# Kernel tuning notes

Measured on AMD Instinct MI355X. Metric: run time of the kernel, lower is better.

Reference implementation:

```python
import jax, jax.numpy as jnp
import numpy as np

N = 32768      # nodes
E = 524288     # edges (avg degree 16)
F = 64         # node_feat_dim
D = 64         # gnn_dim (= per-head out channels, concat=False)
ED = 32        # edge_feat_dim
L = 6          # num_layers
H = 2          # heads
C = D          # per-head channels
LN_EPS = 1e-5


def layer_norm(h, g, b):
    mu = jnp.mean(h, axis=-1, keepdims=True)
    var = jnp.mean((h - mu) ** 2, axis=-1, keepdims=True)
    return g * (h - mu) * jax.lax.rsqrt(var + LN_EPS) + b


def setup_inputs() -> dict:
    key = jax.random.key(0)
    ks = jax.random.split(key, 16)
    x = jax.random.normal(ks[0], (N, F), jnp.float32)
    edge_index = jax.random.randint(ks[1], (2, E), 0, N, jnp.int32)
    edge_attr = jax.random.normal(ks[2], (E, ED), jnp.float32)
    manual_gamma = 1.0 + 0.1 * jax.random.normal(ks[3], (L, D), jnp.float32)
    manual_beta = 0.1 * jax.random.normal(ks[4], (L, D), jnp.float32)
    # node_embed Linear(F, D)
    embed_W = jax.random.normal(ks[5], (F, D), jnp.float32) / np.float32(np.sqrt(F))
    embed_b = jnp.zeros((D,), jnp.float32)
    # per-layer LayerNorm affine params
    ln_gamma = jnp.ones((L, D), jnp.float32)
    ln_beta = jnp.zeros((L, D), jnp.float32)
    # per-layer GATConv params (shared lin for src/dst, PyG non-bipartite)
    lin_W = jax.random.normal(ks[6], (L, D, H * C), jnp.float32) / np.float32(np.sqrt(D))
    lin_edge_W = jax.random.normal(ks[7], (L, ED, H * C), jnp.float32) / np.float32(np.sqrt(ED))
    att_src = jax.random.normal(ks[8], (L, H, C), jnp.float32) / np.float32(np.sqrt(C))
    att_dst = jax.random.normal(ks[9], (L, H, C), jnp.float32) / np.float32(np.sqrt(C))
    att_edge = jax.random.normal(ks[10], (L, H, C), jnp.float32) / np.float32(np.sqrt(C))
    gat_bias = jnp.zeros((L, C), jnp.float32)
    # edge output head: Linear(2D+ED, D) -> ReLU -> Linear(D, 1)
    head_W1 = jax.random.normal(ks[11], (2 * D + ED, D), jnp.float32) / np.float32(np.sqrt(2 * D + ED))
    head_b1 = jnp.zeros((D,), jnp.float32)
    head_W2 = jax.random.normal(ks[12], (D, 1), jnp.float32) / np.float32(np.sqrt(D))
    head_b2 = jnp.zeros((1,), jnp.float32)
    return dict(x=x, edge_index=edge_index, edge_attr=edge_attr,
                manual_gamma=manual_gamma, manual_beta=manual_beta,
                embed_W=embed_W, embed_b=embed_b, ln_gamma=ln_gamma, ln_beta=ln_beta,
                lin_W=lin_W, lin_edge_W=lin_edge_W, att_src=att_src, att_dst=att_dst,
                att_edge=att_edge, gat_bias=gat_bias, head_W1=head_W1, head_b1=head_b1,
                head_W2=head_W2, head_b2=head_b2)


def reference(x, edge_index, edge_attr, manual_gamma, manual_beta,
              embed_W, embed_b, ln_gamma, ln_beta, lin_W, lin_edge_W,
              att_src, att_dst, att_edge, gat_bias, head_W1, head_b1,
              head_W2, head_b2):
    src, dst = edge_index[0], edge_index[1]
    # PyG GATConv default add_self_loops=True, fill_value='mean' for edge_attr
    loop = jnp.arange(N, dtype=edge_index.dtype)
    src_f = jnp.concatenate([src, loop])   # [E+N]
    dst_f = jnp.concatenate([dst, loop])
    deg = jax.ops.segment_sum(jnp.ones((E,), x.dtype), dst, num_segments=N)
    loop_attr = jax.ops.segment_sum(edge_attr, dst, num_segments=N) / jnp.maximum(deg, 1.0)[:, None]
    edge_attr_f = jnp.concatenate([edge_attr, loop_attr], axis=0)  # [E+N, ED]

    h = x @ embed_W + embed_b  # [N, D]
    for l in range(L):
        hn = layer_norm(h, ln_gamma[l], ln_beta[l])
        hm = manual_gamma[l][None, :] * hn + manual_beta[l][None, :]
        xh = (hm @ lin_W[l]).reshape(N, H, C)                      # [N,H,C]
        a_s = jnp.sum(xh * att_src[l][None], axis=-1)              # [N,H]
        a_d = jnp.sum(xh * att_dst[l][None], axis=-1)              # [N,H]
        eh = (edge_attr_f @ lin_edge_W[l]).reshape(-1, H, C)       # [E+N,H,C]
        a_e = jnp.sum(eh * att_edge[l][None], axis=-1)             # [E+N,H]
        alpha = jax.nn.leaky_relu(a_s[src_f] + a_d[dst_f] + a_e, 0.2)
        amax = jax.ops.segment_max(alpha, dst_f, num_segments=N)   # every node has a self-loop
        ex = jnp.exp(alpha - amax[dst_f])
        den = jax.ops.segment_sum(ex, dst_f, num_segments=N)
        w = ex / (den[dst_f] + 1e-16)                              # segment softmax [E+N,H]
        msg = xh[src_f] * w[..., None]                             # [E+N,H,C]
        out = jax.ops.segment_sum(msg, dst_f, num_segments=N)      # [N,H,C]
        h = jax.nn.relu(jnp.mean(out, axis=1) + gat_bias[l])       # concat=False -> head mean

    ef = jnp.concatenate([h[src], h[dst], edge_attr], axis=-1)     # [E, 2D+ED]
    hid = jax.nn.relu(ef @ head_W1 + head_b1)
    return (hid @ head_W2 + head_b2)[:, 0]                         # [E]
```

## Files before the change

kernel.cpp:

```cpp
#include <hip/hip_runtime.h>
#include <hip/hip_bf16.h>
#include <math.h>

#define NN 32768
#define EE 524288
#define LL 6

typedef __attribute__((ext_vector_type(8))) short short8;
typedef __attribute__((ext_vector_type(4))) float floatx4;

union U16x8 { short8 v; unsigned short u[8]; };

__device__ __forceinline__ unsigned short f2bf(float x) {
    union { float f; unsigned int u; } v; v.f = x;
    unsigned int r = v.u + 0x7fffu + ((v.u >> 16) & 1u);
    return (unsigned short)(r >> 16);
}
__device__ __forceinline__ float bf2f(unsigned short h) {
    union { unsigned int u; float f; } v; v.u = (unsigned int)h << 16;
    return v.f;
}


__global__ __launch_bounds__(1024) void scan_kernel(const int* __restrict__ deg,
                                                    int* __restrict__ row_ptr,
                                                    int* __restrict__ cnt) {
    __shared__ int bs[1024];
    int t = threadIdx.x;
    int base = t * 32;
    int loc[32];
    int s = 0;
#pragma unroll
    for (int i = 0; i < 32; ++i) { int v = deg[base + i]; loc[i] = s; s += v; }
    bs[t] = s;
    __syncthreads();
    for (int off = 1; off < 1024; off <<= 1) {
        int v = (t >= off) ? bs[t - off] : 0;
        __syncthreads();
        bs[t] += v;
        __syncthreads();
    }
    int pre = (t == 0) ? 0 : bs[t - 1];
#pragma unroll
    for (int i = 0; i < 32; ++i) { row_ptr[base + i] = pre + loc[i]; cnt[base + i] = 0; }
    if (t == 1023) row_ptr[NN] = bs[1023];
}

__global__ void fill_kernel(const int* __restrict__ src, const int* __restrict__ dst,
                            const int* __restrict__ row_ptr, int* __restrict__ cnt,
                            int2* __restrict__ sedge) {
    int e = blockIdx.x * 256 + threadIdx.x;
    if (e >= EE) return;
    int d = dst[e];
    int pos = row_ptr[d] + atomicAdd(&cnt[d], 1);
    sedge[pos] = make_int2(src[e], e);
}

__global__ __launch_bounds__(256) void smallprep_kernel(
    const float* __restrict__ lin_W, const float* __restrict__ head_W1,
    const float* __restrict__ lin_edge_W, const float* __restrict__ att_edge,
    const float* __restrict__ att_src, const float* __restrict__ att_dst,
    unsigned short* __restrict__ gBhi, unsigned short* __restrict__ gBlo,
    float* __restrict__ vbuf, float* __restrict__ vs, float* __restrict__ vvd,
    unsigned short* __restrict__ w1chi, unsigned short* __restrict__ w1clo) {
    int bb = blockIdx.x;
    int tid = threadIdx.x;
    if (bb < 7) {
        unsigned short* dh = gBhi + (size_t)bb * 128 * 64;
        unsigned short* dl = gBlo + (size_t)bb * 128 * 64;
        if (bb < 6) {
            int n2 = tid & 63, kh = tid >> 6;
            U16x8 hh[4], ll[4];
            for (int kk = 0; kk < 32; ++kk) {
                int j = kh * 32 + kk;
                int h = j >> 6, k = j & 63;
                float wv = 0.5f * lin_W[((size_t)bb * 64 + k) * 128 + h * 64 + n2];
                unsigned short h16 = f2bf(wv);
                hh[kk >> 3].u[kk & 7] = h16;
                ll[kk >> 3].u[kk & 7] = f2bf(wv - bf2f(h16));
            }
#pragma unroll
            for (int c = 0; c < 4; ++c) {
                int cg = kh * 4 + c;
                int off = n2 * 128 + ((cg ^ (n2 & 15)) << 3);
                *(short8*)(dh + off) = hh[c].v;
                *(short8*)(dl + off) = ll[c].v;
            }
        } else {
            int n = tid & 127, kh = tid >> 7;
            U16x8 hh[4], ll[4];
            for (int kk = 0; kk < 32; ++kk) {
                int k = kh * 32 + kk;
                float wv = (n < 64) ? head_W1[k * 64 + n] : head_W1[(64 + k) * 64 + (n - 64)];
                unsigned short h16 = f2bf(wv);
                hh[kk >> 3].u[kk & 7] = h16;
                ll[kk >> 3].u[kk & 7] = f2bf(wv - bf2f(h16));
            }
#pragma unroll
            for (int c = 0; c < 4; ++c) {
                int cg = kh * 4 + c;
                int off = n * 64 + ((cg ^ (n & 7)) << 3);
                *(short8*)(dh + off) = hh[c].v;
                *(short8*)(dl + off) = ll[c].v;
            }
        }
    } else if (bb == 7) {
        for (int t = tid; t < 384; t += 256) {
            int l = t / 64; int r = t & 63; int ed = r >> 1; int hh = r & 1;
            const float* w = lin_edge_W + l * 32 * 128 + ed * 128 + hh * 64;
            const float* a = att_edge + l * 128 + hh * 64;
            float s = 0.f;
#pragma unroll 8
            for (int c = 0; c < 64; ++c) s += w[c] * a[c];
            vbuf[t] = s;
        }
        int n = tid & 63, kc = tid >> 6;
#pragma unroll
        for (int j = 0; j < 8; ++j) {
            int k = kc * 8 + j;
            float wv = head_W1[(128 + k) * 64 + n];
            unsigned short h16 = f2bf(wv);
            w1chi[n * 32 + k] = h16;
            w1clo[n * 32 + k] = f2bf(wv - bf2f(h16));
        }
    } else {
        int l = bb - 8;
        int sel = tid >> 7, idx = tid & 127;
        int h = idx >> 6, k = idx & 63;
        const float* att = (sel ? att_dst : att_src) + l * 128 + h * 64;
        const float* wr = lin_W + ((size_t)l * 64 + k) * 128 + h * 64;
        float s = 0.f;
#pragma unroll 8
        for (int c = 0; c < 64; ++c) s += wr[c] * att[c];
        (sel ? vvd : vs)[l * 128 + idx] = s;
    }
}

__global__ void ae_deg_kernel(const float* __restrict__ edge_attr,
                              const int* __restrict__ dst,
                              const float* __restrict__ v,
                              float* __restrict__ aeo,
                              unsigned short* __restrict__ eabf,
                              int* __restrict__ deg) {
    __shared__ float sv[384];
    int tid = threadIdx.x;
    for (int i = tid; i < 384; i += 128) sv[i] = v[i];
    __syncthreads();
    int e = blockIdx.x * 128 + tid;
    if (e >= EE) return;
    atomicAdd(&deg[dst[e]], 1);
    float ea[32];
    const float4* p = (const float4*)(edge_attr + (size_t)e * 32);
#pragma unroll
    for (int i = 0; i < 8; ++i) {
        float4 f = p[i];
        ea[4 * i] = f.x; ea[4 * i + 1] = f.y; ea[4 * i + 2] = f.z; ea[4 * i + 3] = f.w;
    }
    U16x8 ub[4];
#pragma unroll
    for (int j = 0; j < 32; ++j) ub[j >> 3].u[j & 7] = f2bf(ea[j]);
#pragma unroll
    for (int j = 0; j < 4; ++j) *(short8*)(eabf + (size_t)e * 32 + j * 8) = ub[j].v;
#pragma unroll
    for (int l = 0; l < LL; ++l) {
        float s0 = 0.f, s1 = 0.f;
#pragma unroll
        for (int ed = 0; ed < 32; ++ed) {
            float x = ea[ed];
            s0 += x * sv[l * 64 + ed * 2];
            s1 += x * sv[l * 64 + ed * 2 + 1];
        }
        aeo[((size_t)l * EE + e) * 2] = s0;
        aeo[((size_t)l * EE + e) * 2 + 1] = s1;
    }
}

__global__ __launch_bounds__(256) void embed_ln_kernel(
    const float* __restrict__ x, const float* __restrict__ W, const float* __restrict__ b,
    const float* __restrict__ ln_g, const float* __restrict__ ln_b,
    const float* __restrict__ mg, const float* __restrict__ mb,
    const float* __restrict__ vs0, const float* __restrict__ vd0,
    unsigned short* __restrict__ hm_bf, float* __restrict__ a_s, float* __restrict__ a_d) {
    __shared__ float xr[4][64];
    int w = threadIdx.x >> 6, j = threadIdx.x & 63;
    int n = blockIdx.x * 4 + w;
    xr[w][j] = x[(size_t)n * 64 + j];
    __syncthreads();
    float acc = b[j];
#pragma unroll 8
    for (int k = 0; k < 64; ++k) acc += xr[w][k] * W[k * 64 + j];
    float s = acc, sq = acc * acc;
    for (int off = 1; off < 64; off <<= 1) { s += __shfl_xor(s, off); sq += __shfl_xor(sq, off); }
    float mu = s * (1.f / 64.f);
    float var = sq * (1.f / 64.f) - mu * mu;
    float rs = rsqrtf(var + 1e-5f);
    float hm = mg[j] * (ln_g[j] * (acc - mu) * rs + ln_b[j]) + mb[j];
    hm_bf[(size_t)n * 64 + j] = f2bf(hm);
    float s0 = hm * vs0[j], s1 = hm * vs0[64 + j];
    float d0 = hm * vd0[j], d1 = hm * vd0[64 + j];
    for (int off = 1; off < 64; off <<= 1) {
        s0 += __shfl_xor(s0, off); s1 += __shfl_xor(s1, off);
        d0 += __shfl_xor(d0, off); d1 += __shfl_xor(d1, off);
    }
    if (j == 0) {
        a_s[n * 2] = s0; a_s[n * 2 + 1] = s1;
        a_d[n * 2] = d0; a_d[n * 2 + 1] = d1;
    }
}

__device__ __forceinline__ void fma8(uint4 pv, float w0, float w1, float* a0, float* a1) {
    unsigned int u[4] = {pv.x, pv.y, pv.z, pv.w};
#pragma unroll
    for (int j = 0; j < 4; ++j) {
        union { unsigned int q; float f; } lo, hi;
        lo.q = u[j] << 16; hi.q = u[j] & 0xffff0000u;
        a0[2 * j] += w0 * lo.f;  a1[2 * j] += w1 * lo.f;
        a0[2 * j + 1] += w0 * hi.f;  a1[2 * j + 1] += w1 * hi.f;
    }
}

__global__ __launch_bounds__(256) void aggregate6_kernel(
    const unsigned short* __restrict__ hm_bf, const float* __restrict__ a_s,
    const float* __restrict__ a_d, const float* __restrict__ aeo,
    const int* __restrict__ row_ptr, const int2* __restrict__ sedge,
    unsigned short* __restrict__ Abf) {
    int w = threadIdx.x >> 6, lane = threadIdx.x & 63;
    int n = blockIdx.x * 4 + w;
    int slot = lane >> 3, ch = lane & 7;
    const float2* as2 = (const float2*)a_s;
    const float2* ae2 = (const float2*)aeo;
    const uint4* hmv = (const uint4*)hm_bf;
    float2 adn = ((const float2*)a_d)[n];
    float2 asn = as2[n];
    uint4 pvself = hmv[(size_t)n * 8 + ch];
    int beg = row_ptr[n], end = row_ptr[n + 1];

    float acc0[8] = {}, acc1[8] = {};
    float den0 = 0.f, den1 = 0.f, aex = 0.f, aey = 0.f;

    for (int cs = beg; cs < end; cs += 64) {
        int cnt = min(64, end - cs);
        float w0v = 0.f, w1v = 0.f;
        int sval = n;
        if (lane < cnt) {
            int2 se = sedge[cs + lane];
            float2 ae = ae2[se.y];
            float2 as = as2[se.x];
            aex += ae.x; aey += ae.y;
            float al0 = as.x + adn.x + ae.x; al0 = al0 > 0.f ? al0 : 0.2f * al0;
            float al1 = as.y + adn.y + ae.y; al1 = al1 > 0.f ? al1 : 0.2f * al1;
            w0v = __expf(al0);
            w1v = __expf(al1);
            sval = se.x;
        }
        int ng2 = (cnt + 15) >> 4;
        for (int g2 = 0; g2 < ng2; ++g2) {
            int eA = g2 * 16 + slot, eB = eA + 8;
            int svA = __shfl(sval, eA), svB = __shfl(sval, eB);
            float wA0 = __shfl(w0v, eA), wA1 = __shfl(w1v, eA);
            float wB0 = __shfl(w0v, eB), wB1 = __shfl(w1v, eB);
            uint4 pvA = hmv[(size_t)svA * 8 + ch];
            uint4 pvB = hmv[(size_t)svB * 8 + ch];
            fma8(pvA, wA0, wA1, acc0, acc1);
            den0 += wA0; den1 += wA1;
            fma8(pvB, wB0, wB1, acc0, acc1);
            den0 += wB0; den1 += wB1;
        }
    }
    for (int m = 1; m < 8; m <<= 1) {
        aex += __shfl_xor(aex, m);
        aey += __shfl_xor(aey, m);
    }
#pragma unroll
    for (int m = 8; m < 64; m <<= 1) {
#pragma unroll
        for (int j = 0; j < 8; ++j) {
            acc0[j] += __shfl_xor(acc0[j], m);
            acc1[j] += __shfl_xor(acc1[j], m);
        }
        den0 += __shfl_xor(den0, m);
        den1 += __shfl_xor(den1, m);
        aex += __shfl_xor(aex, m);
        aey += __shfl_xor(aey, m);
    }
    if (slot == 0) {
        float invd = 1.f / fmaxf((float)(end - beg), 1.f);
        float al0 = asn.x + adn.x + aex * invd; al0 = al0 > 0.f ? al0 : 0.2f * al0;
        float al1 = asn.y + adn.y + aey * invd; al1 = al1 > 0.f ? al1 : 0.2f * al1;
        float ws0 = __expf(al0), ws1 = __expf(al1);
        fma8(pvself, ws0, ws1, acc0, acc1);
        den0 += ws0; den1 += ws1;
        float inv0 = 1.f / (den0 + 1e-16f), inv1 = 1.f / (den1 + 1e-16f);
        U16x8 h0, h1;
#pragma unroll
        for (int j = 0; j < 8; ++j) {
            h0.u[j] = f2bf(acc0[j] * inv0);
            h1.u[j] = f2bf(acc1[j] * inv1);
        }
        int i15 = n & 15;
        unsigned short* row = Abf + (size_t)n * 128;
        *(short8*)(row + ((ch ^ i15) << 3)) = h0.v;
        *(short8*)(row + (((8 + ch) ^ i15) << 3)) = h1.v;
    }
}

__global__ __launch_bounds__(256) void post_gemm(
    const unsigned short* __restrict__ Abf, const unsigned short* __restrict__ gBhi,
    const unsigned short* __restrict__ gBlo, const float* __restrict__ bias,
    const float* __restrict__ ln_g, const float* __restrict__ ln_b,
    const float* __restrict__ mg, const float* __restrict__ mb,
    const float* __restrict__ vsn, const float* __restrict__ vdn,
    unsigned short* __restrict__ hm_bf, float* __restrict__ a_s, float* __restrict__ a_d) {
    __shared__ unsigned short Ahi[64 * 128];
    __shared__ unsigned short Bhi[64 * 128], Blo[64 * 128];
    int tid = threadIdx.x;
    {
        const uint4* sa = (const uint4*)(Abf + (size_t)blockIdx.x * 64 * 128);
        const uint4* sh = (const uint4*)gBhi;
        const uint4* sl = (const uint4*)gBlo;
        for (int i = tid; i < 1024; i += 256) {
            ((uint4*)Ahi)[i] = sa[i];
            ((uint4*)Bhi)[i] = sh[i];
            ((uint4*)Blo)[i] = sl[i];
        }
    }
    __syncthreads();

    int w = tid >> 6, lane = tid & 63, col = lane & 15, quad = lane >> 4;
    int m = w * 16 + col;
    floatx4 acc[4] = {};
#pragma unroll
    for (int s = 0; s < 4; ++s) {
        int ca = (quad + 4 * s) ^ col;
        short8 ahi = *(const short8*)(Ahi + m * 128 + ca * 8);
#pragma unroll
        for (int t = 0; t < 4; ++t) {
            int off = (t * 16 + col) * 128 + ca * 8;
            short8 bhi = *(const short8*)(Bhi + off);
            short8 blo = *(const short8*)(Blo + off);
            acc[t] = __builtin_amdgcn_mfma_f32_16x16x32_bf16(ahi, blo, acc[t], 0, 0, 0);
            acc[t] = __builtin_amdgcn_mfma_f32_16x16x32_bf16(ahi, bhi, acc[t], 0, 0, 0);
        }
    }
    int nodebase = blockIdx.x * 64 + w * 16;
    float bv[4];
#pragma unroll
    for (int t = 0; t < 4; ++t) bv[t] = bias[t * 16 + col];
    float vsv[4], vsv1[4], vdv[4], vdv1[4], lg[4], lb[4], mgv[4], mbv[4];
#pragma unroll
    for (int t = 0; t < 4; ++t) {
        int c = t * 16 + col;
        vsv[t] = vsn[c]; vsv1[t] = vsn[64 + c];
        vdv[t] = vdn[c]; vdv1[t] = vdn[64 + c];
        lg[t] = ln_g[c]; lb[t] = ln_b[c];
        mgv[t] = mg[c]; mbv[t] = mb[c];
    }
#pragma unroll
    for (int r = 0; r < 4; ++r) {
        int node = nodebase + quad * 4 + r;
        float hv[4];
        float s = 0.f, sq = 0.f;
#pragma unroll
        for (int t = 0; t < 4; ++t) {
            float v = acc[t][r] + bv[t];
            v = v > 0.f ? v : 0.f;
            hv[t] = v;
            s += v; sq += v * v;
        }
        for (int off = 1; off < 16; off <<= 1) { s += __shfl_xor(s, off); sq += __shfl_xor(sq, off); }
        float mu = s * (1.f / 64.f);
        float var = sq * (1.f / 64.f) - mu * mu;
        float rs = rsqrtf(var + 1e-5f);
        float s0 = 0.f, s1 = 0.f, d0 = 0.f, d1 = 0.f;
#pragma unroll
        for (int t = 0; t < 4; ++t) {
            float hmv = mgv[t] * (lg[t] * (hv[t] - mu) * rs + lb[t]) + mbv[t];
            hm_bf[(size_t)node * 64 + t * 16 + col] = f2bf(hmv);
            s0 += hmv * vsv[t]; s1 += hmv * vsv1[t];
            d0 += hmv * vdv[t]; d1 += hmv * vdv1[t];
        }
        for (int off = 1; off < 16; off <<= 1) {
            s0 += __shfl_xor(s0, off); s1 += __shfl_xor(s1, off);
            d0 += __shfl_xor(d0, off); d1 += __shfl_xor(d1, off);
        }
        if (col == 0) {
            a_s[node * 2] = s0; a_s[node * 2 + 1] = s1;
            a_d[node * 2] = d0; a_d[node * 2 + 1] = d1;
        }
    }
}

__global__ __launch_bounds__(256) void postuv_gemm(
    const unsigned short* __restrict__ Abf, const unsigned short* __restrict__ gB5hi,
    const unsigned short* __restrict__ gB5lo, const float* __restrict__ bias,
    const unsigned short* __restrict__ gB6hi, const unsigned short* __restrict__ gB6lo,
    unsigned short* __restrict__ uv) {
    __shared__ unsigned short lds[24576];
    unsigned short* Ahi  = lds;
    unsigned short* B5hi = lds + 8192;
    unsigned short* B5lo = lds + 16384;
    unsigned short* A2hi = lds;
    unsigned short* A2lo = lds + 4096;
    unsigned short* B6hi = lds + 8192;
    unsigned short* B6lo = lds + 16384;
    int tid = threadIdx.x;
    {
        const uint4* sa = (const uint4*)(Abf + (size_t)blockIdx.x * 64 * 128);
        const uint4* sh = (const uint4*)gB5hi;
        const uint4* sl = (const uint4*)gB5lo;
        for (int i = tid; i < 1024; i += 256) {
            ((uint4*)Ahi)[i] = sa[i];
            ((uint4*)B5hi)[i] = sh[i];
            ((uint4*)B5lo)[i] = sl[i];
        }
    }
    __syncthreads();

    int w = tid >> 6, lane = tid & 63, col = lane & 15, quad = lane >> 4;
    int m = w * 16 + col;
    floatx4 acc[4] = {};
#pragma unroll
    for (int s = 0; s < 4; ++s) {
        int ca = (quad + 4 * s) ^ col;
        short8 ahi = *(const short8*)(Ahi + m * 128 + ca * 8);
#pragma unroll
        for (int t = 0; t < 4; ++t) {
            int off = (t * 16 + col) * 128 + ca * 8;
            short8 bhi = *(const short8*)(B5hi + off);
            short8 blo = *(const short8*)(B5lo + off);
            acc[t] = __builtin_amdgcn_mfma_f32_16x16x32_bf16(ahi, blo, acc[t], 0, 0, 0);
            acc[t] = __builtin_amdgcn_mfma_f32_16x16x32_bf16(ahi, bhi, acc[t], 0, 0, 0);
        }
    }
    float bv[4];
#pragma unroll
    for (int t = 0; t < 4; ++t) bv[t] = bias[t * 16 + col];
    __syncthreads();
#pragma unroll
    for (int t = 0; t < 4; ++t) {
        int c = t * 16 + col;
        int cg = c >> 3, cr = c & 7;
#pragma unroll
        for (int r = 0; r < 4; ++r) {
            float v = acc[t][r] + bv[t];
            v = v > 0.f ? v : 0.f;
            int i = w * 16 + quad * 4 + r;
            int off = i * 64 + ((cg ^ (i & 7)) << 3) + cr;
            unsigned short hh = f2bf(v);
            A2hi[off] = hh;
            A2lo[off] = f2bf(v - bf2f(hh));
        }
    }
    for (int i = tid; i < 1024; i += 256) {
        ((uint4*)B6hi)[i] = ((const uint4*)gB6hi)[i];
        ((uint4*)B6lo)[i] = ((const uint4*)gB6lo)[i];
    }
    __syncthreads();

    floatx4 acc2[8] = {};
#pragma unroll
    for (int s = 0; s < 2; ++s) {
        int ca = (quad + 4 * s) ^ (col & 7);
        short8 a2h = *(const short8*)(A2hi + m * 64 + ca * 8);
        short8 a2l = *(const short8*)(A2lo + m * 64 + ca * 8);
#pragma unroll
        for (int t = 0; t < 8; ++t) {
            int off = (t * 16 + col) * 64 + ca * 8;
            short8 bh = *(const short8*)(B6hi + off);
            short8 bl = *(const short8*)(B6lo + off);
            acc2[t] = __builtin_amdgcn_mfma_f32_16x16x32_bf16(a2l, bh, acc2[t], 0, 0, 0);
            acc2[t] = __builtin_amdgcn_mfma_f32_16x16x32_bf16(a2h, bl, acc2[t], 0, 0, 0);
            acc2[t] = __builtin_amdgcn_mfma_f32_16x16x32_bf16(a2h, bh, acc2[t], 0, 0, 0);
        }
    }
    int nodebase = blockIdx.x * 64 + w * 16;
#pragma unroll
    for (int t = 0; t < 8; ++t)
#pragma unroll
        for (int r = 0; r < 4; ++r)
            uv[(size_t)(nodebase + quad * 4 + r) * 128 + t * 16 + col] = f2bf(acc2[t][r]);
}

__global__ __launch_bounds__(256) void head2_kernel(
    const unsigned short* __restrict__ uv, const int* __restrict__ src,
    const int* __restrict__ dst, const unsigned short* __restrict__ eabf,
    const unsigned short* __restrict__ w1chi, const unsigned short* __restrict__ w1clo,
    const float* __restrict__ b1, const float* __restrict__ W2,
    const float* __restrict__ b2, float* __restrict__ out) {
    __shared__ float g[64][68];
    __shared__ unsigned short Abf[64 * 40];
    __shared__ unsigned short Bh[64 * 40], Bl[64 * 40];
    __shared__ int sA[64], dA[64];
    int tid = threadIdx.x;
    int base = blockIdx.x * 64;
    if (tid < 64) sA[tid] = src[base + tid];
    else if (tid < 128) dA[tid - 64] = dst[base + tid - 64];
    {
        int n = tid >> 2, c = tid & 3;
        *(short8*)(Bh + n * 40 + c * 8) = *(const short8*)(w1chi + n * 32 + c * 8);
        *(short8*)(Bl + n * 40 + c * 8) = *(const short8*)(w1clo + n * 32 + c * 8);
    }
    {
        int e = tid >> 2, q = tid & 3;
        *(short8*)(Abf + e * 40 + q * 8) = *(const short8*)(eabf + (size_t)(base + e) * 32 + q * 8);
    }
    __syncthreads();
    {
        int e = tid >> 2, q = tid & 3;
        const uint4* su = (const uint4*)(uv + (size_t)sA[e] * 128);
        const uint4* dv = (const uint4*)(uv + (size_t)dA[e] * 128);
        uint4 U0 = su[2 * q], U1 = su[2 * q + 1];
        uint4 V0 = dv[8 + 2 * q], V1 = dv[9 + 2 * q];
        const float4* b1p = (const float4*)(b1 + q * 16);
        float bb[16];
#pragma unroll
        for (int j = 0; j < 4; ++j) {
            float4 b4 = b1p[j];
            bb[4 * j] = b4.x; bb[4 * j + 1] = b4.y; bb[4 * j + 2] = b4.z; bb[4 * j + 3] = b4.w;
        }
        unsigned int uw[8] = {U0.x, U0.y, U0.z, U0.w, U1.x, U1.y, U1.z, U1.w};
        unsigned int vw[8] = {V0.x, V0.y, V0.z, V0.w, V1.x, V1.y, V1.z, V1.w};
        float* gr = &g[e][q * 16];
#pragma unroll
        for (int j = 0; j < 8; ++j) {
            gr[2 * j] = bf2f((unsigned short)(uw[j] & 0xffff)) +
                        bf2f((unsigned short)(vw[j] & 0xffff)) + bb[2 * j];
            gr[2 * j + 1] = bf2f((unsigned short)(uw[j] >> 16)) +
                            bf2f((unsigned short)(vw[j] >> 16)) + bb[2 * j + 1];
        }
    }
    __syncthreads();

    int lane = tid & 63, w = tid >> 6, col = lane & 15, quad = lane >> 4;
    short8 a = *(const short8*)(Abf + (w * 16 + col) * 40 + quad * 8);
    floatx4 acc[4] = {};
#pragma unroll
    for (int t = 0; t < 4; ++t) {
        int off = (t * 16 + col) * 40 + quad * 8;
        short8 bh = *(const short8*)(Bh + off);
        short8 bl = *(const short8*)(Bl + off);
        acc[t] = __builtin_amdgcn_mfma_f32_16x16x32_bf16(a, bl, acc[t], 0, 0, 0);
        acc[t] = __builtin_amdgcn_mfma_f32_16x16x32_bf16(a, bh, acc[t], 0, 0, 0);
    }
    float sv[4] = {0.f, 0.f, 0.f, 0.f};
#pragma unroll
    for (int t = 0; t < 4; ++t) {
        float w2v = W2[t * 16 + col];
#pragma unroll
        for (int r = 0; r < 4; ++r) {
            float hid = acc[t][r] + g[w * 16 + quad * 4 + r][t * 16 + col];
            hid = hid > 0.f ? hid : 0.f;
            sv[r] += hid * w2v;
        }
    }
    float b2v = b2[0];
#pragma unroll
    for (int r = 0; r < 4; ++r) {
        float v = sv[r];
        v += __shfl_xor(v, 1);
        v += __shfl_xor(v, 2);
        v += __shfl_xor(v, 4);
        v += __shfl_xor(v, 8);
        if (col == 0) out[base + w * 16 + quad * 4 + r] = v + b2v;
    }
}


extern "C" void kernel_launch(void* const* d_in, const int* in_sizes, int n_in,
                              void* d_out, int out_size, void* d_ws, size_t ws_size,
                              hipStream_t stream) {
    const float* x            = (const float*)d_in[0];
    const int*   edge_index   = (const int*)d_in[1];
    const float* edge_attr    = (const float*)d_in[2];
    const float* manual_gamma = (const float*)d_in[3];
    const float* manual_beta  = (const float*)d_in[4];
    const float* embed_W      = (const float*)d_in[5];
    const float* embed_b      = (const float*)d_in[6];
    const float* ln_gamma     = (const float*)d_in[7];
    const float* ln_beta      = (const float*)d_in[8];
    const float* lin_W        = (const float*)d_in[9];
    const float* lin_edge_W   = (const float*)d_in[10];
    const float* att_src      = (const float*)d_in[11];
    const float* att_dst      = (const float*)d_in[12];
    const float* att_edge     = (const float*)d_in[13];
    const float* gat_bias     = (const float*)d_in[14];
    const float* head_W1      = (const float*)d_in[15];
    const float* head_b1      = (const float*)d_in[16];
    const float* head_W2      = (const float*)d_in[17];
    const float* head_b2      = (const float*)d_in[18];
    float* out = (float*)d_out;

    const int* src = edge_index;
    const int* dst = edge_index + EE;

    char* ws = (char*)d_ws;
    size_t off = 0;
    auto alloc = [&](size_t bytes) {
        void* p = ws + off;
        off += (bytes + 255) & ~(size_t)255;
        return p;
    };
    int*   deg        = (int*)alloc(NN * 4);
    int*   row_ptr    = (int*)alloc((NN + 1) * 4);
    int*   cnt        = (int*)alloc(NN * 4);
    int2*  sedge      = (int2*)alloc((size_t)EE * 8);
    float* aeo        = (float*)alloc((size_t)LL * EE * 2 * 4);
    float* vbuf       = (float*)alloc(LL * 64 * 4);
    float* vs         = (float*)alloc(LL * 128 * 4);
    float* vvd        = (float*)alloc(LL * 128 * 4);
    float* a_s        = (float*)alloc((size_t)NN * 2 * 4);
    float* a_d        = (float*)alloc((size_t)NN * 2 * 4);
    unsigned short* Abf   = (unsigned short*)alloc((size_t)NN * 128 * 2);
    unsigned short* hm_bf = (unsigned short*)alloc((size_t)NN * 64 * 2);
    unsigned short* uvbuf = (unsigned short*)alloc((size_t)NN * 128 * 2);
    unsigned short* eabf  = (unsigned short*)alloc((size_t)EE * 32 * 2);
    unsigned short* gBhi  = (unsigned short*)alloc((size_t)7 * 128 * 64 * 2);
    unsigned short* gBlo  = (unsigned short*)alloc((size_t)7 * 128 * 64 * 2);
    unsigned short* w1chi = (unsigned short*)alloc(64 * 32 * 2);
    unsigned short* w1clo = (unsigned short*)alloc(64 * 32 * 2);
    if (off > ws_size) return;

    hipMemsetAsync(deg, 0, NN * 4, stream);

    smallprep_kernel<<<14, 256, 0, stream>>>(lin_W, head_W1, lin_edge_W, att_edge,
                                             att_src, att_dst, gBhi, gBlo, vbuf,
                                             vs, vvd, w1chi, w1clo);
    ae_deg_kernel<<<EE / 128, 128, 0, stream>>>(edge_attr, dst, vbuf, aeo, eabf, deg);
    scan_kernel<<<1, 1024, 0, stream>>>(deg, row_ptr, cnt);
    fill_kernel<<<EE / 256, 256, 0, stream>>>(src, dst, row_ptr, cnt, sedge);
    embed_ln_kernel<<<NN / 4, 256, 0, stream>>>(x, embed_W, embed_b, ln_gamma, ln_beta,
                                                manual_gamma, manual_beta, vs, vvd,
                                                hm_bf, a_s, a_d);

    for (int l = 0; l < LL; ++l) {
        aggregate6_kernel<<<NN / 4, 256, 0, stream>>>(
            hm_bf, a_s, a_d, aeo + (size_t)l * EE * 2, row_ptr, sedge, Abf);
        if (l < LL - 1) {
            post_gemm<<<NN / 64, 256, 0, stream>>>(
                Abf, gBhi + (size_t)l * 128 * 64, gBlo + (size_t)l * 128 * 64,
                gat_bias + l * 64, ln_gamma + (l + 1) * 64, ln_beta + (l + 1) * 64,
                manual_gamma + (l + 1) * 64, manual_beta + (l + 1) * 64,
                vs + (l + 1) * 128, vvd + (l + 1) * 128, hm_bf, a_s, a_d);
        } else {
            postuv_gemm<<<NN / 64, 256, 0, stream>>>(
                Abf, gBhi + (size_t)l * 128 * 64, gBlo + (size_t)l * 128 * 64,
                gat_bias + l * 64, gBhi + (size_t)6 * 128 * 64,
                gBlo + (size_t)6 * 128 * 64, uvbuf);
        }
    }

    head2_kernel<<<EE / 64, 256, 0, stream>>>(uvbuf, src, dst, eabf, w1chi, w1clo,
                                              head_b1, head_W2, head_b2, out);
}
```

Measured before the change: 511.9 us.

## Compute edge attention logits with split-bf16 MFMA and aggregate four nodes per wave

The per-edge attention-logit precompute in ae_deg_kernel moves from scalar FMAs to three bf16 MFMA ops on hi/lo split operands, with the small weight matrix packed in smallprep. The aggregation kernel now assigns 16 lanes per destination node, so one wave handles four nodes, each lane covers one head by 8 channels, and the cross-slot shuffle reduction goes away. This aims to cut idle lanes on low-degree nodes and reduce reduction overhead. In exchange, the wave loops to the maximum degree among its four nodes, and the split-bf16 MFMA adds small numeric differences.

```diff
diff --git a/kernel.cpp b/kernel.cpp
--- a/kernel.cpp
+++ b/kernel.cpp
@@ -61,8 +61,10 @@
     const float* __restrict__ lin_edge_W, const float* __restrict__ att_edge,
     const float* __restrict__ att_src, const float* __restrict__ att_dst,
     unsigned short* __restrict__ gBhi, unsigned short* __restrict__ gBlo,
-    float* __restrict__ vbuf, float* __restrict__ vs, float* __restrict__ vvd,
+    unsigned short* __restrict__ aeBhi, unsigned short* __restrict__ aeBlo,
+    float* __restrict__ vs, float* __restrict__ vvd,
     unsigned short* __restrict__ w1chi, unsigned short* __restrict__ w1clo) {
+    __shared__ float svb[384];
     int bb = blockIdx.x;
     int tid = threadIdx.x;
     if (bb < 7) {
@@ -112,7 +114,7 @@
             float s = 0.f;
 #pragma unroll 8
             for (int c = 0; c < 64; ++c) s += w[c] * a[c];
-            vbuf[t] = s;
+            svb[t] = s;
         }
         int n = tid & 63, kc = tid >> 6;
 #pragma unroll
@@ -122,6 +124,21 @@
             unsigned short h16 = f2bf(wv);
             w1chi[n * 32 + k] = h16;
             w1clo[n * 32 + k] = f2bf(wv - bf2f(h16));
+        }
+        __syncthreads();
+        if (tid < 64) {
+            int n2 = tid & 15, q = tid >> 4;
+            U16x8 hi, lo;
+#pragma unroll
+            for (int i = 0; i < 8; ++i) {
+                int k = q * 8 + i;
+                float val = (n2 < 12) ? svb[(n2 >> 1) * 64 + k * 2 + (n2 & 1)] : 0.f;
+                unsigned short h16 = f2bf(val);
+                hi.u[i] = h16;
+                lo.u[i] = f2bf(val - bf2f(h16));
+            }
+            *(short8*)(aeBhi + tid * 8) = hi.v;
+            *(short8*)(aeBlo + tid * 8) = lo.v;
         }
     } else {
         int l = bb - 8;
@@ -136,42 +153,45 @@
     }
 }
 
-__global__ void ae_deg_kernel(const float* __restrict__ edge_attr,
-                              const int* __restrict__ dst,
-                              const float* __restrict__ v,
-                              float* __restrict__ aeo,
-                              unsigned short* __restrict__ eabf,
-                              int* __restrict__ deg) {
-    __shared__ float sv[384];
+__global__ __launch_bounds__(256) void ae_deg_kernel(
+    const float* __restrict__ edge_attr, const int* __restrict__ dst,
+    const unsigned short* __restrict__ aeBhi, const unsigned short* __restrict__ aeBlo,
+    float* __restrict__ aeo, unsigned short* __restrict__ eabf, int* __restrict__ deg) {
     int tid = threadIdx.x;
-    for (int i = tid; i < 384; i += 128) sv[i] = v[i];
-    __syncthreads();
-    int e = blockIdx.x * 128 + tid;
-    if (e >= EE) return;
+    int w = tid >> 6, lane = tid & 63;
+    int e0 = blockIdx.x * 256 + w * 64;
+    int e = blockIdx.x * 256 + tid;
     atomicAdd(&deg[dst[e]], 1);
-    float ea[32];
-    const float4* p = (const float4*)(edge_attr + (size_t)e * 32);
-#pragma unroll
-    for (int i = 0; i < 8; ++i) {
-        float4 f = p[i];
-        ea[4 * i] = f.x; ea[4 * i + 1] = f.y; ea[4 * i + 2] = f.z; ea[4 * i + 3] = f.w;
-    }
-    U16x8 ub[4];
-#pragma unroll
-    for (int j = 0; j < 32; ++j) ub[j >> 3].u[j & 7] = f2bf(ea[j]);
-#pragma unroll
-    for (int j = 0; j < 4; ++j) *(short8*)(eabf + (size_t)e * 32 + j * 8) = ub[j].v;
-#pragma unroll
-    for (int l = 0; l < LL; ++l) {
-        float s0 = 0.f, s1 = 0.f;
-#pragma unroll
-        for (int ed = 0; ed < 32; ++ed) {
-            float x = ea[ed];
-            s0 += x * sv[l * 64 + ed * 2];
-            s1 += x * sv[l * 64 + ed * 2 + 1];
-        }
-        aeo[((size_t)l * EE + e) * 2] = s0;
-        aeo[((size_t)l * EE + e) * 2 + 1] = s1;
+    short8 bhi = *(const short8*)(aeBhi + lane * 8);
+    short8 blo = *(const short8*)(aeBlo + lane * 8);
+    int r = lane & 15, q = lane >> 4;
+#pragma unroll
+    for (int t = 0; t < 4; ++t) {
+        int er = e0 + t * 16 + r;
+        const float4* p = (const float4*)(edge_attr + (size_t)er * 32 + q * 8);
+        float4 f0 = p[0], f1 = p[1];
+        float av[8] = {f0.x, f0.y, f0.z, f0.w, f1.x, f1.y, f1.z, f1.w};
+        U16x8 hi, lo;
+#pragma unroll
+        for (int jj = 0; jj < 8; ++jj) {
+            unsigned short h16 = f2bf(av[jj]);
+            hi.u[jj] = h16;
+            lo.u[jj] = f2bf(av[jj] - bf2f(h16));
+        }
+        *(short8*)(eabf + (size_t)er * 32 + q * 8) = hi.v;
+        floatx4 acc = {};
+        acc = __builtin_amdgcn_mfma_f32_16x16x32_bf16(lo.v, bhi, acc, 0, 0, 0);
+        acc = __builtin_amdgcn_mfma_f32_16x16x32_bf16(hi.v, blo, acc, 0, 0, 0);
+        acc = __builtin_amdgcn_mfma_f32_16x16x32_bf16(hi.v, bhi, acc, 0, 0, 0);
+        if (r < 12) {
+            int l = r >> 1, h = r & 1;
+            float* dstp = aeo + (size_t)l * EE * 2 + h;
+#pragma unroll
+            for (int rr = 0; rr < 4; ++rr) {
+                int ee2 = e0 + t * 16 + q * 4 + rr;
+                dstp[(size_t)ee2 * 2] = acc[rr];
+            }
+        }
     }
 }
 
@@ -208,25 +228,26 @@
     }
 }
 
-__device__ __forceinline__ void fma8(uint4 pv, float w0, float w1, float* a0, float* a1) {
+__device__ __forceinline__ void fma8h(uint4 pv, float w, float* a) {
     unsigned int u[4] = {pv.x, pv.y, pv.z, pv.w};
 #pragma unroll
-    for (int j = 0; j < 4; ++j) {
-        union { unsigned int q; float f; } lo, hi;
-        lo.q = u[j] << 16; hi.q = u[j] & 0xffff0000u;
-        a0[2 * j] += w0 * lo.f;  a1[2 * j] += w1 * lo.f;
-        a0[2 * j + 1] += w0 * hi.f;  a1[2 * j + 1] += w1 * hi.f;
-    }
-}
-
-__global__ __launch_bounds__(256) void aggregate6_kernel(
+    for (int q = 0; q < 4; ++q) {
+        union { unsigned int x; float f; } lo, hi;
+        lo.x = u[q] << 16; hi.x = u[q] & 0xffff0000u;
+        a[2 * q]     += w * lo.f;
+        a[2 * q + 1] += w * hi.f;
+    }
+}
+
+__global__ __launch_bounds__(256) void aggregate7_kernel(
     const unsigned short* __restrict__ hm_bf, const float* __restrict__ a_s,
     const float* __restrict__ a_d, const float* __restrict__ aeo,
     const int* __restrict__ row_ptr, const int2* __restrict__ sedge,
     unsigned short* __restrict__ Abf) {
     int w = threadIdx.x >> 6, lane = threadIdx.x & 63;
-    int n = blockIdx.x * 4 + w;
-    int slot = lane >> 3, ch = lane & 7;
+    int g = lane >> 4, j = lane & 15;
+    int ch = j & 7, hh = j >> 3;
+    int n = blockIdx.x * 16 + w * 4 + g;
     const float2* as2 = (const float2*)a_s;
     const float2* ae2 = (const float2*)aeo;
     const uint4* hmv = (const uint4*)hm_bf;
@@ -234,16 +255,25 @@
     float2 asn = as2[n];
     uint4 pvself = hmv[(size_t)n * 8 + ch];
     int beg = row_ptr[n], end = row_ptr[n + 1];
-
-    float acc0[8] = {}, acc1[8] = {};
-    float den0 = 0.f, den1 = 0.f, aex = 0.f, aey = 0.f;
-
-    for (int cs = beg; cs < end; cs += 64) {
-        int cnt = min(64, end - cs);
+    int degn = end - beg;
+
+    float acc[8] = {};
+    float den = 0.f, aex = 0.f, aey = 0.f;
+    int gbase = g << 4;
+
+    int niter = (degn + 15) >> 4;
+    {
+        int o = __shfl_xor(niter, 16); niter = niter > o ? niter : o;
+        o = __shfl_xor(niter, 32); niter = niter > o ? niter : o;
+    }
+    for (int it = 0; it < niter; ++it) {
+        int cs = beg + (it << 4);
+        int rem = end - cs;
+        rem = rem > 16 ? 16 : rem;
         float w0v = 0.f, w1v = 0.f;
         int sval = n;
-        if (lane < cnt) {
-            int2 se = sedge[cs + lane];
+        if (j < rem) {
+            int2 se = sedge[cs + j];
             float2 ae = ae2[se.y];
             float2 as = as2[se.x];
             aex += ae.x; aey += ae.y;
@@ -253,55 +283,39 @@
             w1v = __expf(al1);
             sval = se.x;
         }
-        int ng2 = (cnt + 15) >> 4;
-        for (int g2 = 0; g2 < ng2; ++g2) {
-            int eA = g2 * 16 + slot, eB = eA + 8;
-            int svA = __shfl(sval, eA), svB = __shfl(sval, eB);
-            float wA0 = __shfl(w0v, eA), wA1 = __shfl(w1v, eA);
-            float wB0 = __shfl(w0v, eB), wB1 = __shfl(w1v, eB);
-            uint4 pvA = hmv[(size_t)svA * 8 + ch];
-            uint4 pvB = hmv[(size_t)svB * 8 + ch];
-            fma8(pvA, wA0, wA1, acc0, acc1);
-            den0 += wA0; den1 += wA1;
-            fma8(pvB, wB0, wB1, acc0, acc1);
-            den0 += wB0; den1 += wB1;
-        }
-    }
-    for (int m = 1; m < 8; m <<= 1) {
+        int r2 = rem > 0 ? rem : 0;
+        {
+            int o = __shfl_xor(r2, 16); r2 = r2 > o ? r2 : o;
+            o = __shfl_xor(r2, 32); r2 = r2 > o ? r2 : o;
+        }
+        for (int s = 0; s < r2; ++s) {
+            int idx = gbase + s;
+            int sb = __shfl(sval, idx);
+            float wb0 = __shfl(w0v, idx);
+            float wb1 = __shfl(w1v, idx);
+            float wb = hh ? wb1 : wb0;
+            uint4 pv = hmv[(size_t)sb * 8 + ch];
+            den += wb;
+            fma8h(pv, wb, acc);
+        }
+    }
+#pragma unroll
+    for (int m = 1; m < 16; m <<= 1) {
         aex += __shfl_xor(aex, m);
         aey += __shfl_xor(aey, m);
     }
-#pragma unroll
-    for (int m = 8; m < 64; m <<= 1) {
-#pragma unroll
-        for (int j = 0; j < 8; ++j) {
-            acc0[j] += __shfl_xor(acc0[j], m);
-            acc1[j] += __shfl_xor(acc1[j], m);
-        }
-        den0 += __shfl_xor(den0, m);
-        den1 += __shfl_xor(den1, m);
-        aex += __shfl_xor(aex, m);
-        aey += __shfl_xor(aey, m);
-    }
-    if (slot == 0) {
-        float invd = 1.f / fmaxf((float)(end - beg), 1.f);
-        float al0 = asn.x + adn.x + aex * invd; al0 = al0 > 0.f ? al0 : 0.2f * al0;
-        float al1 = asn.y + adn.y + aey * invd; al1 = al1 > 0.f ? al1 : 0.2f * al1;
-        float ws0 = __expf(al0), ws1 = __expf(al1);
-        fma8(pvself, ws0, ws1, acc0, acc1);
-        den0 += ws0; den1 += ws1;
-        float inv0 = 1.f / (den0 + 1e-16f), inv1 = 1.f / (den1 + 1e-16f);
-        U16x8 h0, h1;
-#pragma unroll
-        for (int j = 0; j < 8; ++j) {
-            h0.u[j] = f2bf(acc0[j] * inv0);
-            h1.u[j] = f2bf(acc1[j] * inv1);
-        }
-        int i15 = n & 15;
-        unsigned short* row = Abf + (size_t)n * 128;
-        *(short8*)(row + ((ch ^ i15) << 3)) = h0.v;
-        *(short8*)(row + (((8 + ch) ^ i15) << 3)) = h1.v;
-    }
+    float invd = 1.f / fmaxf((float)degn, 1.f);
+    float al0 = asn.x + adn.x + aex * invd; al0 = al0 > 0.f ? al0 : 0.2f * al0;
+    float al1 = asn.y + adn.y + aey * invd; al1 = al1 > 0.f ? al1 : 0.2f * al1;
+    float ws = hh ? __expf(al1) : __expf(al0);
+    den += ws;
+    fma8h(pvself, ws, acc);
+    float inv = 1.f / (den + 1e-16f);
+    U16x8 hb;
+#pragma unroll
+    for (int q = 0; q < 8; ++q) hb.u[q] = f2bf(acc[q] * inv);
+    int cg = hh * 8 + ch;
+    *(short8*)(Abf + (size_t)n * 128 + ((cg ^ (n & 15)) << 3)) = hb.v;
 }
 
 __global__ __launch_bounds__(256) void post_gemm(
@@ -605,7 +619,6 @@
     int*   cnt        = (int*)alloc(NN * 4);
     int2*  sedge      = (int2*)alloc((size_t)EE * 8);
     float* aeo        = (float*)alloc((size_t)LL * EE * 2 * 4);
-    float* vbuf       = (float*)alloc(LL * 64 * 4);
     float* vs         = (float*)alloc(LL * 128 * 4);
     float* vvd        = (float*)alloc(LL * 128 * 4);
     float* a_s        = (float*)alloc((size_t)NN * 2 * 4);
@@ -618,14 +631,16 @@
     unsigned short* gBlo  = (unsigned short*)alloc((size_t)7 * 128 * 64 * 2);
     unsigned short* w1chi = (unsigned short*)alloc(64 * 32 * 2);
     unsigned short* w1clo = (unsigned short*)alloc(64 * 32 * 2);
+    unsigned short* aeBhi = (unsigned short*)alloc(64 * 8 * 2);
+    unsigned short* aeBlo = (unsigned short*)alloc(64 * 8 * 2);
     if (off > ws_size) return;
 
     hipMemsetAsync(deg, 0, NN * 4, stream);
 
     smallprep_kernel<<<14, 256, 0, stream>>>(lin_W, head_W1, lin_edge_W, att_edge,
-                                             att_src, att_dst, gBhi, gBlo, vbuf,
+                                             att_src, att_dst, gBhi, gBlo, aeBhi, aeBlo,
                                              vs, vvd, w1chi, w1clo);
-    ae_deg_kernel<<<EE / 128, 128, 0, stream>>>(edge_attr, dst, vbuf, aeo, eabf, deg);
+    ae_deg_kernel<<<EE / 256, 256, 0, stream>>>(edge_attr, dst, aeBhi, aeBlo, aeo, eabf, deg);
     scan_kernel<<<1, 1024, 0, stream>>>(deg, row_ptr, cnt);
     fill_kernel<<<EE / 256, 256, 0, stream>>>(src, dst, row_ptr, cnt, sedge);
     embed_ln_kernel<<<NN / 4, 256, 0, stream>>>(x, embed_W, embed_b, ln_gamma, ln_beta,
@@ -633,7 +648,7 @@
                                                 hm_bf, a_s, a_d);
 
     for (int l = 0; l < LL; ++l) {
-        aggregate6_kernel<<<NN / 4, 256, 0, stream>>>(
+        aggregate7_kernel<<<NN / 16, 256, 0, stream>>>(
             hm_bf, a_s, a_d, aeo + (size_t)l * EE * 2, row_ptr, sedge, Abf);
         if (l < LL - 1) {
             post_gemm<<<NN / 64, 256, 0, stream>>>(
```

After: 477.3 us. 6.8% less time.
